# Performance work log

Measured on AMD Instinct MI355X. Metric: run time of the kernel, lower is better.

Reference implementation:

```python
import jax, jax.numpy as jnp
import numpy as np

D_MODEL = 2048
NHEADS = 16
ROPE_DIM = 64      # config.rope['head_dim']
NOPE_DIM = 128     # config.nope_head_dim
V_DIM = 128        # config.v_head_dim
Q_LORA = 1536      # config.q_lora_rank
KV_LORA = 512      # config.kv_lora_rank
ROPE_BASE = 10000.0
EPS = 1e-6
Q_HEAD = NOPE_DIM + ROPE_DIM   # 192
KV_HEAD = NOPE_DIM + V_DIM     # 256


def rms_norm(x, w):
    return x * jax.lax.rsqrt(jnp.mean(x * x, axis=-1, keepdims=True) + EPS) * w


def apply_rope(x, offset=0):
    # x: (B, H, T, d); standard rotate-half RoPE, positions offset by past length
    d, t = x.shape[-1], x.shape[2]
    inv_freq = 1.0 / (ROPE_BASE ** (jnp.arange(0, d, 2, dtype=jnp.float32) / d))
    pos = jnp.arange(offset, offset + t, dtype=jnp.float32)
    f = pos[:, None] * inv_freq[None, :]          # (T, d/2)
    cos = jnp.concatenate([jnp.cos(f), jnp.cos(f)], -1).astype(x.dtype)
    sin = jnp.concatenate([jnp.sin(f), jnp.sin(f)], -1).astype(x.dtype)
    x1, x2 = jnp.split(x, 2, axis=-1)
    rot = jnp.concatenate([-x2, x1], -1)
    return x * cos + rot * sin


def setup_inputs() -> dict:
    key = jax.random.key(0)
    ks = jax.random.split(key, 8)
    s = 0.02
    return {
        'x': jax.random.normal(ks[0], (2, 2048, D_MODEL), jnp.float32),
        'q_a_w': jax.random.normal(ks[1], (D_MODEL, Q_LORA), jnp.float32) * s,
        'q_a_norm_w': jnp.ones((Q_LORA,), jnp.float32),
        'q_b_w': jax.random.normal(ks[2], (Q_LORA, NHEADS * Q_HEAD), jnp.float32) * s,
        'kv_a_w': jax.random.normal(ks[3], (D_MODEL, KV_LORA + ROPE_DIM), jnp.float32) * s,
        'kv_norm_w': jnp.ones((KV_LORA,), jnp.float32),
        'kv_b_w': jax.random.normal(ks[4], (KV_LORA, NHEADS * KV_HEAD), jnp.float32) * s,
        'o_w': jax.random.normal(ks[5], (NHEADS * V_DIM, D_MODEL), jnp.float32) * s,
    }


def reference(x, q_a_w, q_a_norm_w, q_b_w, kv_a_w, kv_norm_w, kv_b_w, o_w):
    B, T, _ = x.shape
    # Query: LoRA down-proj -> RMSNorm -> up-proj
    q = rms_norm(x @ q_a_w, q_a_norm_w) @ q_b_w            # (B,T,H*Q_HEAD)
    q = q.reshape(B, T, NHEADS, Q_HEAD).transpose(0, 2, 1, 3)
    q_nope, q_rope = q[..., :NOPE_DIM], q[..., NOPE_DIM:]
    # KV: joint compressed projection, split into latent + shared rope key
    kv = x @ kv_a_w                                         # (B,T,KV_LORA+ROPE_DIM)
    kv_c, k_rope = kv[..., :KV_LORA], kv[..., KV_LORA:]
    k_rope = k_rope[:, None, :, :]                          # (B,1,T,ROPE_DIM) - MQA rope key
    kvb = rms_norm(kv_c, kv_norm_w) @ kv_b_w                # (B,T,H*KV_HEAD)
    kvb = kvb.reshape(B, T, NHEADS, KV_HEAD).transpose(0, 2, 1, 3)
    k_nope, v = kvb[..., :NOPE_DIM], kvb[..., NOPE_DIM:]
    # Decoupled RoPE (prefill: offset 0)
    q_rope = apply_rope(q_rope)
    k_rope = apply_rope(k_rope)
    qs = jnp.concatenate([q_nope, q_rope], -1)              # (B,H,T,Q_HEAD)
    ks = jnp.concatenate([k_nope, jnp.broadcast_to(k_rope, (B, NHEADS, T, ROPE_DIM))], -1)
    # SDPA with causal mask, scale = 1/sqrt(q_head_dim)
    scale = 1.0 / np.sqrt(Q_HEAD).astype(np.float32)
    scores = jnp.einsum('bhqd,bhkd->bhqk', qs, ks) * scale
    mask = jnp.tril(jnp.ones((T, T), bool))
    scores = jnp.where(mask[None, None], scores, jnp.finfo(scores.dtype).min)
    attn = jax.nn.softmax(scores, axis=-1)
    out = jnp.einsum('bhqk,bhkd->bhqd', attn, v)            # (B,H,T,V_DIM)
    out = out.transpose(0, 2, 1, 3).reshape(B, T, NHEADS * V_DIM)
    return out @ o_w                                        # (B,T,d_model)
```

## Files before the change

kernel.cpp:

```cpp
#include <hip/hip_runtime.h>
#include <hip/hip_bf16.h>
#include <math.h>

#define NHEADS 16
#define SEQ 2048
#define BATCH 2
#define NTOK (BATCH * SEQ)
#define EPSF 1e-6f

typedef short bf16x8 __attribute__((ext_vector_type(8)));
typedef float f32x4 __attribute__((ext_vector_type(4)));

__device__ __forceinline__ unsigned short f2bf(float v) {
    __hip_bfloat16 h = __float2bfloat16(v);
    return *reinterpret_cast<unsigned short*>(&h);
}
__device__ __forceinline__ float bf2f(unsigned short u) {
    __hip_bfloat16 h = *reinterpret_cast<__hip_bfloat16*>(&u);
    return __bfloat162float(h);
}
__device__ __forceinline__ void g2l16(const void* g, void* l) {
    __builtin_amdgcn_global_load_lds(
        (const __attribute__((address_space(1))) void*)g,
        (__attribute__((address_space(3))) void*)l, 16, 0, 0);
}

#define ROPE_L2 0.4152410118609203f

struct WSeg { const float* src; unsigned short* dst; int Nw, K, nx, off; };
struct WSegs { WSeg s[5]; };
#define CVT_OFF 15104

__global__ __launch_bounds__(256) void prep_weights(
    WSegs segs, const float* __restrict__ x, unsigned short* __restrict__ x_bf)
{
    const int bid = blockIdx.x;
    const int tid = threadIdx.x;
    if (bid >= CVT_OFF) {
        const int i = (bid - CVT_OFF) * 256 + tid;
        float4 a = ((const float4*)x)[i * 2];
        float4 b = ((const float4*)x)[i * 2 + 1];
        unsigned short o[8] = {f2bf(a.x), f2bf(a.y), f2bf(a.z), f2bf(a.w),
                               f2bf(b.x), f2bf(b.y), f2bf(b.z), f2bf(b.w)};
        *(bf16x8*)(x_bf + (size_t)i * 8) = *(bf16x8*)o;
        return;
    }
    __shared__ float T[32][33];
    int si = 0;
#pragma unroll
    for (int i = 1; i < 5; ++i) si += (bid >= segs.s[i].off) ? 1 : 0;
    const WSeg sg = segs.s[si];
    const int local = bid - sg.off;
    const int bx = local % sg.nx, by = local / sg.nx;
    const int n0 = bx * 32, k0 = by * 32;
    const int r = tid >> 3, c4 = (tid & 7) * 4;
    const bool valid = (n0 < sg.Nw);
    if (valid) {
        float4 v = *(const float4*)(sg.src + (size_t)(k0 + r) * sg.Nw + n0 + c4);
        T[r][c4 + 0] = v.x; T[r][c4 + 1] = v.y; T[r][c4 + 2] = v.z; T[r][c4 + 3] = v.w;
    }
    __syncthreads();
    unsigned short o[4];
#pragma unroll
    for (int j = 0; j < 4; ++j) o[j] = valid ? f2bf(T[c4 + j][r]) : (unsigned short)0;
    *(ulong1*)(sg.dst + (size_t)(n0 + r) * sg.K + k0 + c4) = *(ulong1*)o;
}

template <int OUT_BF16>
__global__ __launch_bounds__(256) void gemm_bt(
    const unsigned short* __restrict__ A,
    const unsigned short* __restrict__ Bt,
    void* __restrict__ Cv,
    int K, int N)
{
    __shared__ __align__(16) unsigned short As[128 * 32];
    __shared__ __align__(16) unsigned short Bs[128 * 32];
    const int tid = threadIdx.x;
    const int lane = tid & 63, wid = tid >> 6;
    const int l16 = lane & 15, lq = lane >> 4;
    const int wr = wid >> 1, wc = wid & 1;
    const int bm = blockIdx.y * 128, bn = blockIdx.x * 128;

    f32x4 acc[4][4];
#pragma unroll
    for (int m = 0; m < 4; ++m)
#pragma unroll
        for (int n = 0; n < 4; ++n) acc[m][n] = (f32x4){0.f, 0.f, 0.f, 0.f};

    for (int k0 = 0; k0 < K; k0 += 32) {
        __syncthreads();
#pragma unroll
        for (int t = 0; t < 2; ++t) {
            const int chunk = t * 256 + tid;
            const int row = chunk >> 2, koff = (chunk & 3) << 3;
            g2l16(A  + (size_t)(bm + row) * K + k0 + koff, (char*)As + chunk * 16);
            g2l16(Bt + (size_t)(bn + row) * K + k0 + koff, (char*)Bs + chunk * 16);
        }
        __syncthreads();

        bf16x8 af[4], bfr[4];
#pragma unroll
        for (int m = 0; m < 4; ++m)
            af[m] = *(const bf16x8*)(As + (wr * 64 + m * 16 + l16) * 32 + lq * 8);
#pragma unroll
        for (int n = 0; n < 4; ++n)
            bfr[n] = *(const bf16x8*)(Bs + (wc * 64 + n * 16 + l16) * 32 + lq * 8);
#pragma unroll
        for (int m = 0; m < 4; ++m)
#pragma unroll
            for (int n = 0; n < 4; ++n)
                acc[m][n] = __builtin_amdgcn_mfma_f32_16x16x32_bf16(af[m], bfr[n], acc[m][n], 0, 0, 0);
    }

#pragma unroll
    for (int m = 0; m < 4; ++m)
#pragma unroll
        for (int n = 0; n < 4; ++n)
#pragma unroll
            for (int reg = 0; reg < 4; ++reg) {
                const int row = bm + wr * 64 + m * 16 + lq * 4 + reg;
                const int col = bn + wc * 64 + n * 16 + l16;
                if (OUT_BF16) ((unsigned short*)Cv)[(size_t)row * N + col] = f2bf(acc[m][n][reg]);
                else          ((float*)Cv)[(size_t)row * N + col] = acc[m][n][reg];
            }
}

__global__ __launch_bounds__(256) void gemm_stage2(
    const unsigned short* __restrict__ qa,
    const unsigned short* __restrict__ wqb,
    unsigned short* __restrict__ qbuf,
    const unsigned short* __restrict__ kvc,
    const unsigned short* __restrict__ wkvb,
    unsigned short* __restrict__ kvb,
    unsigned short* __restrict__ vt)
{
    __shared__ __align__(16) unsigned short As[128 * 32];
    __shared__ __align__(16) unsigned short Bs[128 * 32];
    const int bid = blockIdx.x;
    const int tid = threadIdx.x;
    const int lane = tid & 63, wid = tid >> 6;
    const int l16 = lane & 15, lq = lane >> 4;
    const int wr = wid >> 1, wc = wid & 1;

    const bool is_q = bid < 768;
    const unsigned short* A;
    const unsigned short* Bt;
    int K, N, bm, bn;
    if (is_q) { A = qa;  Bt = wqb;  K = 1536; N = 3072; bn = (bid % 24) * 128;        bm = (bid / 24) * 128; }
    else      { A = kvc; Bt = wkvb; K = 512;  N = 4096; bn = ((bid - 768) % 32) * 128; bm = ((bid - 768) / 32) * 128; }

    f32x4 acc[4][4];
#pragma unroll
    for (int m = 0; m < 4; ++m)
#pragma unroll
        for (int n = 0; n < 4; ++n) acc[m][n] = (f32x4){0.f, 0.f, 0.f, 0.f};

    for (int k0 = 0; k0 < K; k0 += 32) {
        __syncthreads();
#pragma unroll
        for (int t = 0; t < 2; ++t) {
            const int chunk = t * 256 + tid;
            const int row = chunk >> 2, koff = (chunk & 3) << 3;
            g2l16(A  + (size_t)(bm + row) * K + k0 + koff, (char*)As + chunk * 16);
            g2l16(Bt + (size_t)(bn + row) * K + k0 + koff, (char*)Bs + chunk * 16);
        }
        __syncthreads();

        bf16x8 af[4], bfr[4];
#pragma unroll
        for (int m = 0; m < 4; ++m)
            af[m] = *(const bf16x8*)(As + (wr * 64 + m * 16 + l16) * 32 + lq * 8);
#pragma unroll
        for (int n = 0; n < 4; ++n)
            bfr[n] = *(const bf16x8*)(Bs + (wc * 64 + n * 16 + l16) * 32 + lq * 8);
#pragma unroll
        for (int m = 0; m < 4; ++m)
#pragma unroll
            for (int n = 0; n < 4; ++n)
                acc[m][n] = __builtin_amdgcn_mfma_f32_16x16x32_bf16(af[m], bfr[n], acc[m][n], 0, 0, 0);
    }

    const bool is_v = (!is_q) && ((bn & 255) == 128);
    if (!is_v) {
        unsigned short* C = is_q ? qbuf : kvb;
#pragma unroll
        for (int m = 0; m < 4; ++m)
#pragma unroll
            for (int n = 0; n < 4; ++n)
#pragma unroll
                for (int reg = 0; reg < 4; ++reg) {
                    const int row = bm + wr * 64 + m * 16 + lq * 4 + reg;
                    const int col = bn + wc * 64 + n * 16 + l16;
                    C[(size_t)row * N + col] = f2bf(acc[m][n][reg]);
                }
    } else {
        const int h = bn >> 8;
#pragma unroll
        for (int m = 0; m < 4; ++m)
#pragma unroll
            for (int n = 0; n < 4; ++n) {
                const int d = wc * 64 + n * 16 + l16;
                const int tok0 = bm + wr * 64 + m * 16 + lq * 4;
                const int b_ = tok0 >> 11, s_ = tok0 & (SEQ - 1);
                unsigned short pk[4];
#pragma unroll
                for (int reg = 0; reg < 4; ++reg) pk[reg] = f2bf(acc[m][n][reg]);
                *(ulong1*)(vt + (((size_t)(b_ * NHEADS + h) * 128 + d) * SEQ + s_)) = *(ulong1*)pk;
            }
    }
}

__global__ __launch_bounds__(256) void norms_fused(
    const float* __restrict__ qkv, const float* __restrict__ qw,
    const float* __restrict__ kvw,
    unsigned short* __restrict__ qa_out, unsigned short* __restrict__ kv_out,
    unsigned short* __restrict__ krope_out)
{
    const int bid = blockIdx.x;
    const int tid = threadIdx.x;
    __shared__ float wsum[4];
    __shared__ float s_scale;
    const int wave = tid >> 6;

    if (bid < 4096) {
        const int row = bid;
        const float* p = qkv + (size_t)row * 2176;
        float ss = 0.f;
#pragma unroll
        for (int t = 0; t < 6; ++t) { float v = p[tid + t * 256]; ss += v * v; }
#pragma unroll
        for (int off = 32; off > 0; off >>= 1) ss += __shfl_down(ss, off, 64);
        if ((tid & 63) == 0) wsum[wave] = ss;
        __syncthreads();
        if (tid == 0) {
            float t = wsum[0] + wsum[1] + wsum[2] + wsum[3];
            s_scale = rsqrtf(t / 1536.0f + EPSF);
        }
        __syncthreads();
        const float sc = s_scale;
#pragma unroll
        for (int t = 0; t < 6; ++t) {
            int c = tid + t * 256;
            qa_out[(size_t)row * 1536 + c] = f2bf(p[c] * sc * qw[c]);
        }
    } else {
        const int row = bid - 4096;
        const float* p = qkv + (size_t)row * 2176 + 1536;
        float v0 = p[tid], v1 = p[tid + 256];
        float ss = v0 * v0 + v1 * v1;
#pragma unroll
        for (int off = 32; off > 0; off >>= 1) ss += __shfl_down(ss, off, 64);
        if ((tid & 63) == 0) wsum[wave] = ss;
        __syncthreads();
        if (tid == 0) {
            float t = wsum[0] + wsum[1] + wsum[2] + wsum[3];
            s_scale = rsqrtf(t / 512.0f + EPSF);
        }
        __syncthreads();
        const float sc = s_scale;
        kv_out[(size_t)row * 512 + tid]       = f2bf(v0 * sc * kvw[tid]);
        kv_out[(size_t)row * 512 + tid + 256] = f2bf(v1 * sc * kvw[tid + 256]);
        if (tid < 64) {
            const int s = row & (SEQ - 1);
            const int j = tid, jj = j & 31;
            float inv = exp2f(-ROPE_L2 * (float)jj);
            float f = (float)s * inv;
            float sn, cs;
            sincosf(f, &sn, &cs);
            const float* kb = p + 512;
            float v = (j < 32) ? (kb[j] * cs - kb[j + 32] * sn)
                               : (kb[j] * cs + kb[j - 32] * sn);
            krope_out[(size_t)row * 64 + j] = f2bf(v);
        }
    }
}

#define KPD 200
#define VPD 72
#define PPD 72
#define RESCALE_THR 8.0f

__global__ __launch_bounds__(256) void flash_mfma(
    const unsigned short* __restrict__ qbuf,
    const unsigned short* __restrict__ kvb,
    const unsigned short* __restrict__ krope,
    const unsigned short* __restrict__ vt,
    unsigned short* __restrict__ ctx)
{
    __shared__ __align__(16) unsigned short Ks[64][KPD];
    __shared__ __align__(16) unsigned short Vs[144][VPD];
    __shared__ __align__(16) unsigned short Ps[4][16][PPD];
    const int id = blockIdx.x;
    const int xcd = id & 7, sl = id >> 3;
    const int grp = sl >> 4, pair = sl & 15;
    const int hb = xcd + 8 * grp;
    const int h = hb & 15, b = hb >> 4;
    const int tid = threadIdx.x;
    const int wid = tid >> 6, lane = tid & 63;
    const int l16 = lane & 15, lq = lane >> 4;

    const size_t headV = (size_t)(b * NHEADS + h) * 128 * SEQ;
    const float scale = 0.07216878364870323f;

    float cs8[8], sn8[8];
    const int vrow = tid >> 1, vg = tid & 1;

    {
        int r = 128 + (tid >> 4);
        int c = (tid & 15) * 4;
        unsigned short v = (tid >> 4) == 0 ? (unsigned short)0x3F80 : (unsigned short)0;
        Vs[r][c] = v; Vs[r][c + 1] = v; Vs[r][c + 2] = v; Vs[r][c + 3] = v;
    }

#pragma unroll
    for (int pass = 0; pass < 2; ++pass) {
        const int qt = pass ? (31 - pair) : pair;
        const int srow = qt * 64 + wid * 16 + l16;

        bf16x8 qf[6];
        {
            const unsigned short* qp = qbuf + (size_t)(b * SEQ + srow) * 3072 + h * 192 + lq * 8;
            bf16x8 raw[6];
#pragma unroll
            for (int kk = 0; kk < 6; ++kk) raw[kk] = *(const bf16x8*)(qp + kk * 32);
#pragma unroll
            for (int jj = 0; jj < 8; ++jj) {
                float inv = exp2f(-ROPE_L2 * (float)(lq * 8 + jj));
                float fp = (float)srow * inv;
                sn8[jj] = __sinf(fp);
                cs8[jj] = __cosf(fp);
            }
#pragma unroll
            for (int kk = 0; kk < 4; ++kk) {
                unsigned short o[8];
#pragma unroll
                for (int e = 0; e < 8; ++e) o[e] = f2bf(bf2f(((unsigned short*)&raw[kk])[e]) * scale);
                qf[kk] = *(bf16x8*)o;
            }
            unsigned short o4[8], o5[8];
#pragma unroll
            for (int e = 0; e < 8; ++e) {
                float x1 = bf2f(((unsigned short*)&raw[4])[e]);
                float x2 = bf2f(((unsigned short*)&raw[5])[e]);
                o4[e] = f2bf((x1 * cs8[e] - x2 * sn8[e]) * scale);
                o5[e] = f2bf((x2 * cs8[e] + x1 * sn8[e]) * scale);
            }
            qf[4] = *(bf16x8*)o4;
            qf[5] = *(bf16x8*)o5;
        }

        f32x4 o[8];
#pragma unroll
        for (int f = 0; f < 8; ++f) o[f] = (f32x4){0.f, 0.f, 0.f, 0.f};
        f32x4 oS = (f32x4){0.f, 0.f, 0.f, 0.f};
        float m[4] = {-1e30f, -1e30f, -1e30f, -1e30f};

        const int nkt = qt + 1;
        for (int kt = 0; kt < nkt; ++kt) {
            __syncthreads();
            {
                const int tk0 = b * SEQ + kt * 64;
#pragma unroll
                for (int t = 0; t < 4; ++t) {
                    int i = tid + t * 256;
                    int r = i >> 4, c8 = i & 15;
                    *(bf16x8*)&Ks[r][c8 * 8] =
                        *(const bf16x8*)(kvb + (size_t)(tk0 + r) * 4096 + h * 256 + c8 * 8);
                }
#pragma unroll
                for (int t = 0; t < 2; ++t) {
                    int i = tid + t * 256;
                    int r = i >> 3, c8 = i & 7;
                    *(bf16x8*)&Ks[r][128 + c8 * 8] =
                        *(const bf16x8*)(krope + (size_t)(tk0 + r) * 64 + c8 * 8);
                }
                const unsigned short* vsrc = vt + headV + (size_t)vrow * SEQ + kt * 64 + vg * 8;
#pragma unroll
                for (int j = 0; j < 4; ++j)
                    *(bf16x8*)&Vs[vrow][(vg + j * 2) * 8] = *(const bf16x8*)(vsrc + j * 16);
            }
            __syncthreads();

            f32x4 s[4];
#pragma unroll
            for (int f = 0; f < 4; ++f) s[f] = (f32x4){0.f, 0.f, 0.f, 0.f};
            __builtin_amdgcn_s_setprio(1);
#pragma unroll
            for (int f = 0; f < 4; ++f) {
#pragma unroll
                for (int kk = 0; kk < 6; ++kk) {
                    bf16x8 bfr = *(const bf16x8*)&Ks[f * 16 + l16][kk * 32 + lq * 8];
                    s[f] = __builtin_amdgcn_mfma_f32_16x16x32_bf16(qf[kk], bfr, s[f], 0, 0, 0);
                }
            }
            __builtin_amdgcn_s_setprio(0);

            const int qabs = qt * 64 + wid * 16 + lq * 4;
            const bool diag = (kt == qt);
            float rmax4[4];
#pragma unroll
            for (int reg = 0; reg < 4; ++reg) {
                if (diag) {
                    int q = qabs + reg;
                    int k0 = kt * 64 + l16;
                    if (k0      > q) s[0][reg] = -1e30f;
                    if (k0 + 16 > q) s[1][reg] = -1e30f;
                    if (k0 + 32 > q) s[2][reg] = -1e30f;
                    if (k0 + 48 > q) s[3][reg] = -1e30f;
                }
                float rmax = fmaxf(fmaxf(s[0][reg], s[1][reg]), fmaxf(s[2][reg], s[3][reg]));
                rmax = fmaxf(rmax, __shfl_xor(rmax, 1, 64));
                rmax = fmaxf(rmax, __shfl_xor(rmax, 2, 64));
                rmax = fmaxf(rmax, __shfl_xor(rmax, 4, 64));
                rmax = fmaxf(rmax, __shfl_xor(rmax, 8, 64));
                rmax4[reg] = rmax;
            }
            float dmx = fmaxf(fmaxf(rmax4[0] - m[0], rmax4[1] - m[1]),
                              fmaxf(rmax4[2] - m[2], rmax4[3] - m[3]));
            if (!__all(dmx <= RESCALE_THR)) {
#pragma unroll
                for (int reg = 0; reg < 4; ++reg) {
                    float mnew = fmaxf(m[reg], rmax4[reg]);
                    float al = __expf(m[reg] - mnew);
                    m[reg] = mnew;
#pragma unroll
                    for (int f = 0; f < 8; ++f) o[f][reg] *= al;
                    oS[reg] *= al;
                }
            }
#pragma unroll
            for (int reg = 0; reg < 4; ++reg) {
                Ps[wid][lq * 4 + reg][ 0 + l16] = f2bf(__expf(s[0][reg] - m[reg]));
                Ps[wid][lq * 4 + reg][16 + l16] = f2bf(__expf(s[1][reg] - m[reg]));
                Ps[wid][lq * 4 + reg][32 + l16] = f2bf(__expf(s[2][reg] - m[reg]));
                Ps[wid][lq * 4 + reg][48 + l16] = f2bf(__expf(s[3][reg] - m[reg]));
            }

            bf16x8 pa0 = *(const bf16x8*)&Ps[wid][l16][lq * 8];
            bf16x8 pa1 = *(const bf16x8*)&Ps[wid][l16][32 + lq * 8];
            __builtin_amdgcn_s_setprio(1);
#pragma unroll
            for (int f = 0; f < 8; ++f) {
                bf16x8 b0 = *(const bf16x8*)&Vs[f * 16 + l16][lq * 8];
                bf16x8 b1 = *(const bf16x8*)&Vs[f * 16 + l16][32 + lq * 8];
                o[f] = __builtin_amdgcn_mfma_f32_16x16x32_bf16(pa0, b0, o[f], 0, 0, 0);
                o[f] = __builtin_amdgcn_mfma_f32_16x16x32_bf16(pa1, b1, o[f], 0, 0, 0);
            }
            {
                bf16x8 s0 = *(const bf16x8*)&Vs[128 + l16][lq * 8];
                bf16x8 s1 = *(const bf16x8*)&Vs[128 + l16][32 + lq * 8];
                oS = __builtin_amdgcn_mfma_f32_16x16x32_bf16(pa0, s0, oS, 0, 0, 0);
                oS = __builtin_amdgcn_mfma_f32_16x16x32_bf16(pa1, s1, oS, 0, 0, 0);
            }
            __builtin_amdgcn_s_setprio(0);
        }

#pragma unroll
        for (int reg = 0; reg < 4; ++reg) {
            float ls = __shfl(oS[reg], lane & 48, 64);
            float inv = 1.0f / ls;
            unsigned short* dst = ctx + (size_t)(b * SEQ + qt * 64 + wid * 16 + lq * 4 + reg) * 2048 + h * 128 + l16;
#pragma unroll
            for (int f = 0; f < 8; ++f) dst[f * 16] = f2bf(o[f][reg] * inv);
        }
    }
}

extern "C" void kernel_launch(void* const* d_in, const int* in_sizes, int n_in,
                              void* d_out, int out_size, void* d_ws, size_t ws_size,
                              hipStream_t stream) {
    const float* x          = (const float*)d_in[0];
    const float* q_a_w      = (const float*)d_in[1];
    const float* q_a_norm_w = (const float*)d_in[2];
    const float* q_b_w      = (const float*)d_in[3];
    const float* kv_a_w     = (const float*)d_in[4];
    const float* kv_norm_w  = (const float*)d_in[5];
    const float* kv_b_w     = (const float*)d_in[6];
    const float* o_w        = (const float*)d_in[7];
    float* out = (float*)d_out;

    char* ws = (char*)d_ws;
    float*          qkv_cat  = (float*)(ws + 0);
    unsigned short* ctx_bf   = (unsigned short*)(ws + 0);
    unsigned short* qbuf_bf  = (unsigned short*)(ws + 35651584);
    unsigned short* vt_bf    = (unsigned short*)(ws + 60817408);
    unsigned short* kvb_bf   = (unsigned short*)(ws + 77594624);
    unsigned short* x_bf     = (unsigned short*)(ws + 111149056);
    unsigned short* q_a_bf   = (unsigned short*)(ws + 111149056);
    unsigned short* kv_c_bf  = (unsigned short*)(ws + 127926272);
    unsigned short* krope_bf = (unsigned short*)(ws + 132120576);
    unsigned short* wcat     = (unsigned short*)(ws + 132644864);
    unsigned short* wkva_t   = wcat + (size_t)1536 * 2048;
    unsigned short* wqb_t    = (unsigned short*)(ws + 141557760);
    unsigned short* wkvb_t   = (unsigned short*)(ws + 150994944);
    unsigned short* wo_t     = (unsigned short*)(ws + 155189248);

    dim3 blk(256);

    WSegs segs;
    segs.s[0] = { q_a_w,  wcat,   1536, 2048,  48,     0 };
    segs.s[1] = { q_b_w,  wqb_t,  3072, 1536,  96,  3072 };
    segs.s[2] = { kv_a_w, wkva_t,  576, 2048,  20,  7680 };
    segs.s[3] = { kv_b_w, wkvb_t, 4096,  512, 128,  8960 };
    segs.s[4] = { o_w,    wo_t,   2048, 2048,  64, 11008 };
    prep_weights<<<CVT_OFF + 4096, blk, 0, stream>>>(segs, x, x_bf);

    gemm_bt<0><<<dim3(17, 32), blk, 0, stream>>>(x_bf, wcat, qkv_cat, 2048, 2176);

    norms_fused<<<8192, blk, 0, stream>>>(qkv_cat, q_a_norm_w, kv_norm_w,
                                          q_a_bf, kv_c_bf, krope_bf);

    gemm_stage2<<<1792, blk, 0, stream>>>(q_a_bf, wqb_t, qbuf_bf,
                                          kv_c_bf, wkvb_t, kvb_bf, vt_bf);

    flash_mfma<<<dim3(512), blk, 0, stream>>>(qbuf_bf, kvb_bf, krope_bf, vt_bf, ctx_bf);

    gemm_bt<0><<<dim3(16, 32), blk, 0, stream>>>(ctx_bf, wo_t, out, 2048, 2048);
}
```

Baseline: 342.9 us.

## Double-buffer GEMM LDS tiles and adjust flash V/P LDS padding

Both bf16 GEMM kernels now keep two LDS buffers for the A and B tiles. The next K-tile is loaded with global_load_lds while the MFMAs run on the current one, so each iteration needs one barrier instead of two. The V and P LDS row pitches in the flash attention kernel change from 72 to 76 elements to reduce bank conflicts. The cost is double the GEMM LDS use, which may lower occupancy. The 152-byte pitch also breaks 16-byte alignment for vector LDS reads, which may split accesses.

```diff
diff --git a/kernel.cpp b/kernel.cpp
--- a/kernel.cpp
+++ b/kernel.cpp
@@ -66,6 +66,18 @@
     *(ulong1*)(sg.dst + (size_t)(n0 + r) * sg.K + k0 + c4) = *(ulong1*)o;
 }
 
+#define GSTAGE(AS, BS, BUF, T)                                                  \
+    do {                                                                        \
+        const int k0_ = (T) * 32;                                               \
+        _Pragma("unroll")                                                       \
+        for (int t_ = 0; t_ < 2; ++t_) {                                        \
+            const int chunk_ = t_ * 256 + tid;                                  \
+            const int row_ = chunk_ >> 2, koff_ = (chunk_ & 3) << 3;            \
+            g2l16(A  + (size_t)(bm + row_) * K + k0_ + koff_, (char*)AS[BUF] + chunk_ * 16); \
+            g2l16(Bt + (size_t)(bn + row_) * K + k0_ + koff_, (char*)BS[BUF] + chunk_ * 16); \
+        }                                                                       \
+    } while (0)
+
 template <int OUT_BF16>
 __global__ __launch_bounds__(256) void gemm_bt(
     const unsigned short* __restrict__ A,
@@ -73,8 +85,8 @@
     void* __restrict__ Cv,
     int K, int N)
 {
-    __shared__ __align__(16) unsigned short As[128 * 32];
-    __shared__ __align__(16) unsigned short Bs[128 * 32];
+    __shared__ __align__(16) unsigned short As[2][128 * 32];
+    __shared__ __align__(16) unsigned short Bs[2][128 * 32];
     const int tid = threadIdx.x;
     const int lane = tid & 63, wid = tid >> 6;
     const int l16 = lane & 15, lq = lane >> 4;
@@ -87,29 +99,26 @@
 #pragma unroll
         for (int n = 0; n < 4; ++n) acc[m][n] = (f32x4){0.f, 0.f, 0.f, 0.f};
 
-    for (int k0 = 0; k0 < K; k0 += 32) {
+    const int nk = K >> 5;
+    GSTAGE(As, Bs, 0, 0);
+    int cur = 0;
+    for (int t = 0; t < nk; ++t) {
         __syncthreads();
-#pragma unroll
-        for (int t = 0; t < 2; ++t) {
-            const int chunk = t * 256 + tid;
-            const int row = chunk >> 2, koff = (chunk & 3) << 3;
-            g2l16(A  + (size_t)(bm + row) * K + k0 + koff, (char*)As + chunk * 16);
-            g2l16(Bt + (size_t)(bn + row) * K + k0 + koff, (char*)Bs + chunk * 16);
-        }
-        __syncthreads();
+        if (t + 1 < nk) GSTAGE(As, Bs, cur ^ 1, t + 1);
 
         bf16x8 af[4], bfr[4];
 #pragma unroll
         for (int m = 0; m < 4; ++m)
-            af[m] = *(const bf16x8*)(As + (wr * 64 + m * 16 + l16) * 32 + lq * 8);
+            af[m] = *(const bf16x8*)(As[cur] + (wr * 64 + m * 16 + l16) * 32 + lq * 8);
 #pragma unroll
         for (int n = 0; n < 4; ++n)
-            bfr[n] = *(const bf16x8*)(Bs + (wc * 64 + n * 16 + l16) * 32 + lq * 8);
+            bfr[n] = *(const bf16x8*)(Bs[cur] + (wc * 64 + n * 16 + l16) * 32 + lq * 8);
 #pragma unroll
         for (int m = 0; m < 4; ++m)
 #pragma unroll
             for (int n = 0; n < 4; ++n)
                 acc[m][n] = __builtin_amdgcn_mfma_f32_16x16x32_bf16(af[m], bfr[n], acc[m][n], 0, 0, 0);
+        cur ^= 1;
     }
 
 #pragma unroll
@@ -134,8 +143,8 @@
     unsigned short* __restrict__ kvb,
     unsigned short* __restrict__ vt)
 {
-    __shared__ __align__(16) unsigned short As[128 * 32];
-    __shared__ __align__(16) unsigned short Bs[128 * 32];
+    __shared__ __align__(16) unsigned short As[2][128 * 32];
+    __shared__ __align__(16) unsigned short Bs[2][128 * 32];
     const int bid = blockIdx.x;
     const int tid = threadIdx.x;
     const int lane = tid & 63, wid = tid >> 6;
@@ -155,29 +164,26 @@
 #pragma unroll
         for (int n = 0; n < 4; ++n) acc[m][n] = (f32x4){0.f, 0.f, 0.f, 0.f};
 
-    for (int k0 = 0; k0 < K; k0 += 32) {
+    const int nk = K >> 5;
+    GSTAGE(As, Bs, 0, 0);
+    int cur = 0;
+    for (int t = 0; t < nk; ++t) {
         __syncthreads();
-#pragma unroll
-        for (int t = 0; t < 2; ++t) {
-            const int chunk = t * 256 + tid;
-            const int row = chunk >> 2, koff = (chunk & 3) << 3;
-            g2l16(A  + (size_t)(bm + row) * K + k0 + koff, (char*)As + chunk * 16);
-            g2l16(Bt + (size_t)(bn + row) * K + k0 + koff, (char*)Bs + chunk * 16);
-        }
-        __syncthreads();
+        if (t + 1 < nk) GSTAGE(As, Bs, cur ^ 1, t + 1);
 
         bf16x8 af[4], bfr[4];
 #pragma unroll
         for (int m = 0; m < 4; ++m)
-            af[m] = *(const bf16x8*)(As + (wr * 64 + m * 16 + l16) * 32 + lq * 8);
+            af[m] = *(const bf16x8*)(As[cur] + (wr * 64 + m * 16 + l16) * 32 + lq * 8);
 #pragma unroll
         for (int n = 0; n < 4; ++n)
-            bfr[n] = *(const bf16x8*)(Bs + (wc * 64 + n * 16 + l16) * 32 + lq * 8);
+            bfr[n] = *(const bf16x8*)(Bs[cur] + (wc * 64 + n * 16 + l16) * 32 + lq * 8);
 #pragma unroll
         for (int m = 0; m < 4; ++m)
 #pragma unroll
             for (int n = 0; n < 4; ++n)
                 acc[m][n] = __builtin_amdgcn_mfma_f32_16x16x32_bf16(af[m], bfr[n], acc[m][n], 0, 0, 0);
+        cur ^= 1;
     }
 
     const bool is_v = (!is_q) && ((bn & 255) == 128);
@@ -276,8 +282,8 @@
 }
 
 #define KPD 200
-#define VPD 72
-#define PPD 72
+#define VPD 76
+#define PPD 76
 #define RESCALE_THR 8.0f
 
 __global__ __launch_bounds__(256) void flash_mfma(
```

New measurement: 329.8 us. 1.04x faster.
